# Kernel tuning notes

Hardware: AMD Instinct MI355X
Metric: run time of the kernel (lower is better)

Reference implementation:

```python
import jax, jax.numpy as jnp
import numpy as np
import math

P = 7          # patch / kernel size (must be odd for onion-peeling: N = 1+4*m*(m+1) = P*P)
EPS = 1e-6
EPS_W = 0.5

def _ball_dirs():
    u = [np.array([[1.0, 0.0]])]
    s = [np.zeros(1)]
    for k in range(1, P // 2 + 1):
        n = 8 * k
        th = np.linspace(0.0, 2.0 * math.pi * (1.0 - 1.0 / n), n)
        u.append(np.stack([np.cos(th), np.sin(th)], 1))
        s.append(np.full(n, k / (P // 2)))
    return (np.concatenate(u, 0).astype(np.float32), np.concatenate(s).astype(np.float32))

_U, _S = _ball_dirs()  # [N,2], [N], N == P*P == 49

def _forward(x, metric_w, metric_b, proj_w, proj_b):
    B, C, H, W = x.shape
    Hp, Wp = H // P, W // P
    u = jnp.asarray(_U)
    s = jnp.asarray(_S)
    # metric net: strided conv -> 7 params per patch
    params = jax.lax.conv_general_dilated(
        x, metric_w, (P, P), 'VALID',
        dimension_numbers=('NCHW', 'OIHW', 'NCHW')) + metric_b[None, :, None, None]
    v_raw = jnp.moveaxis(params[:, :2], 1, -1)                      # [B,Hp,Wp,2]
    v = v_raw / jnp.maximum(jnp.linalg.norm(v_raw, axis=-1, keepdims=True), 1e-12)
    eig = 2.0 * jax.nn.sigmoid(jnp.moveaxis(params[:, 2:4], 1, -1))  # [B,Hp,Wp,2]
    scale = 0.5 + 1.5 * jax.nn.sigmoid(jnp.moveaxis(params[:, 4:5], 1, -1))
    eig = eig * scale
    vp = jnp.stack([-v[..., 1], v[..., 0]], -1)
    R = jnp.stack([v, vp], -1)                                      # [B,Hp,Wp,2,2] (columns v, v_perp)
    M = R @ (eig[..., None] * jnp.swapaxes(R, -1, -2))              # R diag(eig) R^T
    w = params[:, 5:7]                                              # [B,2,Hp,Wp]
    w = w * (1.0 - EPS_W) * jax.nn.sigmoid(jnp.linalg.norm(w, axis=1, keepdims=True))
    # Finsler-Randers norm F(u) = sqrt(u^T M u + eps) + w.u for all N unit dirs
    quad = jnp.einsum('nj,bhwij,ni->bnhw', u, M, u)                 # [B,N,Hp,Wp]
    drift = jnp.einsum('bihw,ni->bnhw', w, u)
    F_u = jnp.sqrt(quad + EPS) + drift
    y = (u[None, :, :, None, None] / (F_u[:, :, None] + EPS)
         * s[None, :, None, None, None])                            # [B,N,2,Hp,Wp]
    y = y.reshape(B, P, P, 2, Hp, Wp)[:, :, :, ::-1]                # flip last coord pair (x,y)->(y,x)
    gi = jnp.arange(P, dtype=x.dtype) - P // 2
    grid = jnp.stack(jnp.meshgrid(gi, gi, indexing='ij'), -1)       # [P,P,2]
    off = y - grid[None, :, :, :, None, None]                       # [B,P,P,2,Hp,Wp]
    off_y = jnp.transpose(off[:, :, :, 0], (0, 3, 4, 1, 2))         # [B,Hp,Wp,P,P]
    off_x = jnp.transpose(off[:, :, :, 1], (0, 3, 4, 1, 2))
    base_h = (jnp.arange(Hp, dtype=x.dtype) * P)[None, :, None, None, None]
    base_w = (jnp.arange(Wp, dtype=x.dtype) * P)[None, None, :, None, None]
    ki = jnp.arange(P, dtype=x.dtype)
    py = off_y + base_h + ki[None, None, None, :, None]             # sample rows
    px = off_x + base_w + ki[None, None, None, None, :]             # sample cols
    # bilinear sampling with zero padding (torchvision deform_conv2d semantics)
    y0 = jnp.floor(py)
    x0 = jnp.floor(px)
    wy = py - y0
    wx = px - x0

    def gather(yi, xi):
        valid = (yi >= 0) & (yi <= H - 1) & (xi >= 0) & (xi <= W - 1)
        yc = jnp.clip(yi, 0, H - 1).astype(jnp.int32)
        xc = jnp.clip(xi, 0, W - 1).astype(jnp.int32)
        vals = jax.vmap(lambda img, yy, xx: img[:, yy, xx])(x, yc, xc)  # [B,C,Hp,Wp,P,P]
        return vals * valid[:, None].astype(x.dtype)

    sampled = (gather(y0, x0) * ((1 - wy) * (1 - wx))[:, None]
               + gather(y0, x0 + 1) * ((1 - wy) * wx)[:, None]
               + gather(y0 + 1, x0) * (wy * (1 - wx))[:, None]
               + gather(y0 + 1, x0 + 1) * (wy * wx)[:, None])       # [B,C,Hp,Wp,P,P]
    out = jnp.einsum('bchwij,ecij->behw', sampled, proj_w) + proj_b[None, :, None, None]
    return jnp.moveaxis(out.reshape(B, out.shape[1], -1), 1, 2)     # [B, Hp*Wp, E]

def setup_inputs():
    key = jax.random.key(0)
    k0, k1, k2 = jax.random.split(key, 3)
    B, C, H, W, E = 64, 3, 224, 224, 384
    x = jax.random.normal(k0, (B, C, H, W), jnp.float32)
    metric_w = jax.random.normal(k1, (7, C, P, P), jnp.float32) / math.sqrt(C * P * P)
    metric_b = jnp.zeros((7,), jnp.float32)
    proj_w = jax.random.normal(k2, (E, C, P, P), jnp.float32) / (P * math.sqrt(C))
    proj_b = jnp.zeros((E,), jnp.float32)
    return {"x": x, "metric_w": metric_w, "metric_b": metric_b,
            "proj_w": proj_w, "proj_b": proj_b}

def reference(x, metric_w, metric_b, proj_w, proj_b):
    return _forward(x, metric_w, metric_b, proj_w, proj_b)
```

## Files before the change

kernel.cpp:

```cpp
#include <hip/hip_runtime.h>
#include <math.h>

#define PP   7
#define NDIR 49
#define CIN  3
#define KK   147
#define KPAD 160
#define EE   384
#define HH   224
#define WW   224
#define GG   16
#define TB1  256
#define TB2  256
#define SSTR 17

typedef __attribute__((ext_vector_type(8))) __bf16 bf16x8;
typedef __attribute__((ext_vector_type(4))) float  f32x4;

__device__ __forceinline__ float sigmoidf_(float v) {
    return 1.0f / (1.0f + expf(-v));
}

__global__ void pack_pw_kernel(const float* __restrict__ pw, unsigned short* __restrict__ pwB) {
    int idx = blockIdx.x * blockDim.x + threadIdx.x;
    if (idx < EE * KPAD) {
        int e = idx / KPAD;
        int k = idx - e * KPAD;
        float v = (k < KK) ? pw[e * KK + k] : 0.0f;
        __bf16 h = (__bf16)v;
        pwB[idx] = *(unsigned short*)&h;
    }
}

__launch_bounds__(TB1)
__global__ void params_kernel(const float* __restrict__ x,
                              const float* __restrict__ mw,
                              const float* __restrict__ mb,
                              float* __restrict__ der) {
    __shared__ float mws[7 * KK];
    const int t = threadIdx.x;
    for (int i = t; i < 7 * KK; i += TB1) mws[i] = mw[i];
    __syncthreads();

    const int p   = blockIdx.x * TB1 + t;
    const int b   = p >> 10;
    const int rem = p & 1023;
    const int hp  = rem >> 5;
    const int wp  = rem & 31;
    const float* xb = x + (size_t)b * (CIN * HH * WW) + (size_t)(hp * PP) * WW + wp * PP;

    float a0 = mb[0], a1 = mb[1], a2 = mb[2], a3 = mb[3], a4 = mb[4], a5 = mb[5], a6 = mb[6];
    #pragma unroll
    for (int c = 0; c < CIN; ++c) {
        #pragma unroll
        for (int i = 0; i < PP; ++i) {
            const float* row = xb + c * (HH * WW) + i * WW;
            float v[7];
            #pragma unroll
            for (int j = 0; j < PP; ++j) v[j] = row[j];
            const int kb = c * 49 + i * 7;
            #pragma unroll
            for (int j = 0; j < PP; ++j) {
                a0 = fmaf(v[j], mws[0 * KK + kb + j], a0);
                a1 = fmaf(v[j], mws[1 * KK + kb + j], a1);
                a2 = fmaf(v[j], mws[2 * KK + kb + j], a2);
                a3 = fmaf(v[j], mws[3 * KK + kb + j], a3);
                a4 = fmaf(v[j], mws[4 * KK + kb + j], a4);
                a5 = fmaf(v[j], mws[5 * KK + kb + j], a5);
                a6 = fmaf(v[j], mws[6 * KK + kb + j], a6);
            }
        }
    }

    float nrm = sqrtf(a0 * a0 + a1 * a1);
    float inv = 1.0f / fmaxf(nrm, 1e-12f);
    float v0 = a0 * inv, v1 = a1 * inv;
    float e0 = 2.0f * sigmoidf_(a2);
    float e1 = 2.0f * sigmoidf_(a3);
    float sc = 0.5f + 1.5f * sigmoidf_(a4);
    e0 *= sc; e1 *= sc;
    float M00 = e0 * v0 * v0 + e1 * v1 * v1;
    float M01 = (e0 - e1) * v0 * v1;
    float M11 = e0 * v1 * v1 + e1 * v0 * v0;
    float wn  = sqrtf(a5 * a5 + a6 * a6);
    float wsc = 0.5f * sigmoidf_(wn);

    float* dp = der + (size_t)p * 8;
    dp[0] = M00; dp[1] = M01; dp[2] = M11; dp[3] = a5 * wsc; dp[4] = a6 * wsc;
}

__launch_bounds__(TB2)
__global__ void gather_gemm_kernel(const float* __restrict__ x,
                                   const float* __restrict__ derg,
                                   const unsigned short* __restrict__ pwB,
                                   const float* __restrict__ pb,
                                   float* __restrict__ out) {
    __shared__ float der_s[GG][5];
    __shared__ float dirs[NDIR][3];
    __shared__ float samp[KK][SSTR];

    const int t   = threadIdx.x;
    const int blk = blockIdx.x;
    const int b   = blk >> 6;
    const int rem = blk & 63;
    const int hp  = rem >> 1;
    const int wp0 = (rem & 1) * GG;
    const size_t m0 = (size_t)blk * GG;

    const float* xb = x + (size_t)b * (CIN * HH * WW);

    if (t < GG * 5) {
        int g = t / 5, f = t - g * 5;
        der_s[g][f] = derg[(m0 + g) * 8 + f];
    }
    if (t >= 64 && t < 64 + NDIR) {
        int n = t - 64;
        float u0, u1, s;
        if (n == 0)      { u0 = 1.0f; u1 = 0.0f; s = 0.0f; }
        else if (n < 9)  { float th = (float)(n - 1)  * 0.78539816339744831f; u0 = cosf(th); u1 = sinf(th); s = 0.33333334f; }
        else if (n < 25) { float th = (float)(n - 9)  * 0.39269908169872414f; u0 = cosf(th); u1 = sinf(th); s = 0.66666669f; }
        else             { float th = (float)(n - 25) * 0.26179938779914941f; u0 = cosf(th); u1 = sinf(th); s = 1.0f; }
        dirs[n][0] = u0; dirs[n][1] = u1; dirs[n][2] = s;
    }
    __syncthreads();

    for (int item = t; item < GG * NDIR; item += TB2) {
        int g = item / NDIR;
        int n = item - g * NDIR;
        float u0 = dirs[n][0], u1 = dirs[n][1], s = dirs[n][2];
        float M00 = der_s[g][0], M01 = der_s[g][1], M11 = der_s[g][2];
        float w0 = der_s[g][3], w1 = der_s[g][4];
        float quad  = u0 * u0 * M00 + 2.0f * u0 * u1 * M01 + u1 * u1 * M11;
        float drift = w0 * u0 + w1 * u1;
        float F = sqrtf(quad + 1e-6f) + drift;
        float r = s / (F + 1e-6f);
        float py = (float)(hp * PP + 3) + u1 * r;
        float px = (float)((wp0 + g) * PP + 3) + u0 * r;
        float y0f = floorf(py), x0f = floorf(px);
        float y1f = y0f + 1.0f, x1f = x0f + 1.0f;
        float wy = py - y0f, wx = px - x0f;
        bool vy0 = (y0f >= 0.0f) && (y0f <= (float)(HH - 1));
        bool vy1 = (y1f >= 0.0f) && (y1f <= (float)(HH - 1));
        bool vx0 = (x0f >= 0.0f) && (x0f <= (float)(WW - 1));
        bool vx1 = (x1f >= 0.0f) && (x1f <= (float)(WW - 1));
        int iy0 = (int)fminf(fmaxf(y0f, 0.0f), (float)(HH - 1));
        int iy1 = (int)fminf(fmaxf(y1f, 0.0f), (float)(HH - 1));
        int ix0 = (int)fminf(fmaxf(x0f, 0.0f), (float)(WW - 1));
        int ix1 = (int)fminf(fmaxf(x1f, 0.0f), (float)(WW - 1));
        float w00 = (1.0f - wy) * (1.0f - wx);
        float w01 = (1.0f - wy) * wx;
        float w10 = wy * (1.0f - wx);
        float w11 = wy * wx;
        #pragma unroll
        for (int c = 0; c < CIN; ++c) {
            const float* xc = xb + c * (HH * WW);
            float v00 = (vy0 && vx0) ? xc[iy0 * WW + ix0] : 0.0f;
            float v01 = (vy0 && vx1) ? xc[iy0 * WW + ix1] : 0.0f;
            float v10 = (vy1 && vx0) ? xc[iy1 * WW + ix0] : 0.0f;
            float v11 = (vy1 && vx1) ? xc[iy1 * WW + ix1] : 0.0f;
            samp[c * NDIR + n][g] = v00 * w00 + v01 * w01 + v10 * w10 + v11 * w11;
        }
    }
    __syncthreads();

    const int lane = t & 63;
    const int wv   = t >> 6;
    const int nrow = lane & 15;
    const int hi   = lane >> 4;

    bf16x8 afr[5];
    #pragma unroll
    for (int ks = 0; ks < 5; ++ks) {
        #pragma unroll
        for (int j = 0; j < 8; ++j) {
            int k = ks * 32 + hi * 8 + j;
            float v = (k < KK) ? samp[k][nrow] : 0.0f;
            afr[ks][j] = (__bf16)v;
        }
    }

    #pragma unroll
    for (int q = 0; q < 6; ++q) {
        int tile = wv * 6 + q;
        int e    = tile * 16 + nrow;
        const unsigned short* brow = pwB + (size_t)e * KPAD + hi * 8;
        f32x4 acc = {0.0f, 0.0f, 0.0f, 0.0f};
        #pragma unroll
        for (int ks = 0; ks < 5; ++ks) {
            bf16x8 bfr = *(const bf16x8*)&brow[ks * 32];
            acc = __builtin_amdgcn_mfma_f32_16x16x32_bf16(afr[ks], bfr, acc, 0, 0, 0);
        }
        float bias = pb[e];
        #pragma unroll
        for (int r = 0; r < 4; ++r) {
            out[(m0 + hi * 4 + r) * EE + e] = acc[r] + bias;
        }
    }
}

extern "C" void kernel_launch(void* const* d_in, const int* in_sizes, int n_in,
                              void* d_out, int out_size, void* d_ws, size_t ws_size,
                              hipStream_t stream) {
    const float* x  = (const float*)d_in[0];
    const float* mw = (const float*)d_in[1];
    const float* mb = (const float*)d_in[2];
    const float* pw = (const float*)d_in[3];
    const float* pb = (const float*)d_in[4];
    float* out = (float*)d_out;
    float* der = (float*)d_ws;
    unsigned short* pwB = (unsigned short*)((char*)d_ws + (size_t)65536 * 8 * 4);

    const int B = in_sizes[0] / (CIN * HH * WW);
    const int NPATCH = B * 32 * 32;

    pack_pw_kernel<<<(EE * KPAD + 255) / 256, 256, 0, stream>>>(pw, pwB);
    params_kernel<<<NPATCH / TB1, TB1, 0, stream>>>(x, mw, mb, der);
    gather_gemm_kernel<<<B * 64, TB2, 0, stream>>>(x, der, pwB, pb, out);
}
```

Measured before the change: 201.3 us.

## Fuse metric-param conv into gather-GEMM kernel and gather from channel-packed image

Drops the separate params kernel. Each gather-GEMM block now stages its 7-row input strip in shared memory and computes the 7 metric parameters for its 16 patches there, so the per-patch parameter buffer never goes through global memory. When workspace allows, a pre-pass repacks x into an interleaved 4-channel layout, so each bilinear tap becomes one 16-byte load instead of three scattered loads. The cost is an extra full pass over the input (writing about 1.3x its size) and more shared memory per block, which may reduce occupancy.

```diff
diff --git a/kernel.cpp b/kernel.cpp
--- a/kernel.cpp
+++ b/kernel.cpp
@@ -10,9 +10,9 @@
 #define HH   224
 #define WW   224
 #define GG   16
-#define TB1  256
-#define TB2  256
+#define TB   256
 #define SSTR 17
+#define NPX  112
 
 typedef __attribute__((ext_vector_type(8))) __bf16 bf16x8;
 typedef __attribute__((ext_vector_type(4))) float  f32x4;
@@ -32,72 +32,34 @@
     }
 }
 
-__launch_bounds__(TB1)
-__global__ void params_kernel(const float* __restrict__ x,
-                              const float* __restrict__ mw,
-                              const float* __restrict__ mb,
-                              float* __restrict__ der) {
+__global__ void pack_x_kernel(const float* __restrict__ x, float* __restrict__ xp, int npix) {
+    int idx = blockIdx.x * blockDim.x + threadIdx.x;
+    if (idx >= npix) return;
+    int b = idx / (HH * WW);
+    int p = idx - b * (HH * WW);
+    const float* xb = x + (size_t)b * (CIN * HH * WW) + p;
+    f32x4 v;
+    v[0] = xb[0];
+    v[1] = xb[HH * WW];
+    v[2] = xb[2 * HH * WW];
+    v[3] = 0.0f;
+    *(f32x4*)(xp + (size_t)idx * 4) = v;
+}
+
+template<bool PACKED>
+__launch_bounds__(TB)
+__global__ void fused_kernel(const float* __restrict__ x,
+                             const float* __restrict__ xp,
+                             const float* __restrict__ mw,
+                             const float* __restrict__ mb,
+                             const unsigned short* __restrict__ pwB,
+                             const float* __restrict__ pb,
+                             float* __restrict__ out) {
     __shared__ float mws[7 * KK];
-    const int t = threadIdx.x;
-    for (int i = t; i < 7 * KK; i += TB1) mws[i] = mw[i];
-    __syncthreads();
-
-    const int p   = blockIdx.x * TB1 + t;
-    const int b   = p >> 10;
-    const int rem = p & 1023;
-    const int hp  = rem >> 5;
-    const int wp  = rem & 31;
-    const float* xb = x + (size_t)b * (CIN * HH * WW) + (size_t)(hp * PP) * WW + wp * PP;
-
-    float a0 = mb[0], a1 = mb[1], a2 = mb[2], a3 = mb[3], a4 = mb[4], a5 = mb[5], a6 = mb[6];
-    #pragma unroll
-    for (int c = 0; c < CIN; ++c) {
-        #pragma unroll
-        for (int i = 0; i < PP; ++i) {
-            const float* row = xb + c * (HH * WW) + i * WW;
-            float v[7];
-            #pragma unroll
-            for (int j = 0; j < PP; ++j) v[j] = row[j];
-            const int kb = c * 49 + i * 7;
-            #pragma unroll
-            for (int j = 0; j < PP; ++j) {
-                a0 = fmaf(v[j], mws[0 * KK + kb + j], a0);
-                a1 = fmaf(v[j], mws[1 * KK + kb + j], a1);
-                a2 = fmaf(v[j], mws[2 * KK + kb + j], a2);
-                a3 = fmaf(v[j], mws[3 * KK + kb + j], a3);
-                a4 = fmaf(v[j], mws[4 * KK + kb + j], a4);
-                a5 = fmaf(v[j], mws[5 * KK + kb + j], a5);
-                a6 = fmaf(v[j], mws[6 * KK + kb + j], a6);
-            }
-        }
-    }
-
-    float nrm = sqrtf(a0 * a0 + a1 * a1);
-    float inv = 1.0f / fmaxf(nrm, 1e-12f);
-    float v0 = a0 * inv, v1 = a1 * inv;
-    float e0 = 2.0f * sigmoidf_(a2);
-    float e1 = 2.0f * sigmoidf_(a3);
-    float sc = 0.5f + 1.5f * sigmoidf_(a4);
-    e0 *= sc; e1 *= sc;
-    float M00 = e0 * v0 * v0 + e1 * v1 * v1;
-    float M01 = (e0 - e1) * v0 * v1;
-    float M11 = e0 * v1 * v1 + e1 * v0 * v0;
-    float wn  = sqrtf(a5 * a5 + a6 * a6);
-    float wsc = 0.5f * sigmoidf_(wn);
-
-    float* dp = der + (size_t)p * 8;
-    dp[0] = M00; dp[1] = M01; dp[2] = M11; dp[3] = a5 * wsc; dp[4] = a6 * wsc;
-}
-
-__launch_bounds__(TB2)
-__global__ void gather_gemm_kernel(const float* __restrict__ x,
-                                   const float* __restrict__ derg,
-                                   const unsigned short* __restrict__ pwB,
-                                   const float* __restrict__ pb,
-                                   float* __restrict__ out) {
+    __shared__ float dirs[NDIR][3];
+    __shared__ float par_s[GG][8];
     __shared__ float der_s[GG][5];
-    __shared__ float dirs[NDIR][3];
-    __shared__ float samp[KK][SSTR];
+    __shared__ float buf[3136];
 
     const int t   = threadIdx.x;
     const int blk = blockIdx.x;
@@ -106,13 +68,10 @@
     const int hp  = rem >> 1;
     const int wp0 = (rem & 1) * GG;
     const size_t m0 = (size_t)blk * GG;
-
-    const float* xb = x + (size_t)b * (CIN * HH * WW);
-
-    if (t < GG * 5) {
-        int g = t / 5, f = t - g * 5;
-        der_s[g][f] = derg[(m0 + g) * 8 + f];
-    }
+    const int row0 = hp * PP;
+    const int col0 = wp0 * PP;
+
+    for (int i = t; i < 7 * KK; i += TB) mws[i] = mw[i];
     if (t >= 64 && t < 64 + NDIR) {
         int n = t - 64;
         float u0, u1, s;
@@ -122,9 +81,66 @@
         else             { float th = (float)(n - 25) * 0.26179938779914941f; u0 = cosf(th); u1 = sinf(th); s = 1.0f; }
         dirs[n][0] = u0; dirs[n][1] = u1; dirs[n][2] = s;
     }
-    __syncthreads();
-
-    for (int item = t; item < GG * NDIR; item += TB2) {
+
+    if (PACKED) {
+        for (int item = t; item < 7 * NPX; item += TB) {
+            int i = item / NPX, px = item - i * NPX;
+            f32x4 v = *(const f32x4*)(xp + ((size_t)((b * HH + row0 + i) * WW) + col0 + px) * 4);
+            *(f32x4*)&buf[item * 4] = v;
+        }
+    } else {
+        for (int item = t; item < CIN * 7 * NPX; item += TB) {
+            int c = item / (7 * NPX), r2 = item - c * (7 * NPX);
+            int i = r2 / NPX, px = r2 - i * NPX;
+            buf[item] = x[(size_t)b * (CIN * HH * WW) + (size_t)c * (HH * WW)
+                          + (size_t)(row0 + i) * WW + col0 + px];
+        }
+    }
+    __syncthreads();
+
+    if (t < 112) {
+        int prm = t >> 4, g = t & 15;
+        float acc = mb[prm];
+        const float* wrow = &mws[prm * KK];
+        #pragma unroll
+        for (int c = 0; c < CIN; ++c) {
+            #pragma unroll
+            for (int i = 0; i < 7; ++i) {
+                #pragma unroll
+                for (int j = 0; j < 7; ++j) {
+                    float xv = PACKED ? buf[(i * NPX + g * 7 + j) * 4 + c]
+                                      : buf[(c * 7 + i) * NPX + g * 7 + j];
+                    acc = fmaf(xv, wrow[c * 49 + i * 7 + j], acc);
+                }
+            }
+        }
+        par_s[g][prm] = acc;
+    }
+    __syncthreads();
+
+    if (t < GG) {
+        float a0 = par_s[t][0], a1 = par_s[t][1], a2 = par_s[t][2], a3 = par_s[t][3];
+        float a4 = par_s[t][4], a5 = par_s[t][5], a6 = par_s[t][6];
+        float nrm = sqrtf(a0 * a0 + a1 * a1);
+        float inv = 1.0f / fmaxf(nrm, 1e-12f);
+        float v0 = a0 * inv, v1 = a1 * inv;
+        float e0 = 2.0f * sigmoidf_(a2);
+        float e1 = 2.0f * sigmoidf_(a3);
+        float sc = 0.5f + 1.5f * sigmoidf_(a4);
+        e0 *= sc; e1 *= sc;
+        float wn  = sqrtf(a5 * a5 + a6 * a6);
+        float wsc = 0.5f * sigmoidf_(wn);
+        der_s[t][0] = e0 * v0 * v0 + e1 * v1 * v1;
+        der_s[t][1] = (e0 - e1) * v0 * v1;
+        der_s[t][2] = e0 * v1 * v1 + e1 * v0 * v0;
+        der_s[t][3] = a5 * wsc;
+        der_s[t][4] = a6 * wsc;
+    }
+    __syncthreads();
+
+    const float* xb = x + (size_t)b * (CIN * HH * WW);
+    const size_t pbase = (size_t)b * (HH * WW);
+    for (int item = t; item < GG * NDIR; item += TB) {
         int g = item / NDIR;
         int n = item - g * NDIR;
         float u0 = dirs[n][0], u1 = dirs[n][1], s = dirs[n][2];
@@ -134,8 +150,8 @@
         float drift = w0 * u0 + w1 * u1;
         float F = sqrtf(quad + 1e-6f) + drift;
         float r = s / (F + 1e-6f);
-        float py = (float)(hp * PP + 3) + u1 * r;
-        float px = (float)((wp0 + g) * PP + 3) + u0 * r;
+        float py = (float)(row0 + 3) + u1 * r;
+        float px = (float)(col0 + g * PP + 3) + u0 * r;
         float y0f = floorf(py), x0f = floorf(px);
         float y1f = y0f + 1.0f, x1f = x0f + 1.0f;
         float wy = py - y0f, wx = px - x0f;
@@ -151,14 +167,31 @@
         float w01 = (1.0f - wy) * wx;
         float w10 = wy * (1.0f - wx);
         float w11 = wy * wx;
-        #pragma unroll
-        for (int c = 0; c < CIN; ++c) {
-            const float* xc = xb + c * (HH * WW);
-            float v00 = (vy0 && vx0) ? xc[iy0 * WW + ix0] : 0.0f;
-            float v01 = (vy0 && vx1) ? xc[iy0 * WW + ix1] : 0.0f;
-            float v10 = (vy1 && vx0) ? xc[iy1 * WW + ix0] : 0.0f;
-            float v11 = (vy1 && vx1) ? xc[iy1 * WW + ix1] : 0.0f;
-            samp[c * NDIR + n][g] = v00 * w00 + v01 * w01 + v10 * w10 + v11 * w11;
+        if (PACKED) {
+            float c00 = w00 * ((vy0 && vx0) ? 1.0f : 0.0f);
+            float c01 = w01 * ((vy0 && vx1) ? 1.0f : 0.0f);
+            float c10 = w10 * ((vy1 && vx0) ? 1.0f : 0.0f);
+            float c11 = w11 * ((vy1 && vx1) ? 1.0f : 0.0f);
+            f32x4 q00 = *(const f32x4*)(xp + (pbase + (size_t)(iy0 * WW + ix0)) * 4);
+            f32x4 q01 = *(const f32x4*)(xp + (pbase + (size_t)(iy0 * WW + ix1)) * 4);
+            f32x4 q10 = *(const f32x4*)(xp + (pbase + (size_t)(iy1 * WW + ix0)) * 4);
+            f32x4 q11 = *(const f32x4*)(xp + (pbase + (size_t)(iy1 * WW + ix1)) * 4);
+            #pragma unroll
+            for (int c = 0; c < CIN; ++c) {
+                buf[(c * NDIR + n) * SSTR + g] =
+                    q00[c] * c00 + q01[c] * c01 + q10[c] * c10 + q11[c] * c11;
+            }
+        } else {
+            #pragma unroll
+            for (int c = 0; c < CIN; ++c) {
+                const float* xc = xb + c * (HH * WW);
+                float v00 = (vy0 && vx0) ? xc[iy0 * WW + ix0] : 0.0f;
+                float v01 = (vy0 && vx1) ? xc[iy0 * WW + ix1] : 0.0f;
+                float v10 = (vy1 && vx0) ? xc[iy1 * WW + ix0] : 0.0f;
+                float v11 = (vy1 && vx1) ? xc[iy1 * WW + ix1] : 0.0f;
+                buf[(c * NDIR + n) * SSTR + g] =
+                    v00 * w00 + v01 * w01 + v10 * w10 + v11 * w11;
+            }
         }
     }
     __syncthreads();
@@ -174,7 +207,7 @@
         #pragma unroll
         for (int j = 0; j < 8; ++j) {
             int k = ks * 32 + hi * 8 + j;
-            float v = (k < KK) ? samp[k][nrow] : 0.0f;
+            float v = (k < KK) ? buf[k * SSTR + nrow] : 0.0f;
             afr[ks][j] = (__bf16)v;
         }
     }
@@ -207,13 +240,20 @@
     const float* pw = (const float*)d_in[3];
     const float* pb = (const float*)d_in[4];
     float* out = (float*)d_out;
-    float* der = (float*)d_ws;
-    unsigned short* pwB = (unsigned short*)((char*)d_ws + (size_t)65536 * 8 * 4);
+
+    unsigned short* pwB = (unsigned short*)d_ws;
+    float* xp = (float*)((char*)d_ws + (size_t)(1 << 17));
 
     const int B = in_sizes[0] / (CIN * HH * WW);
-    const int NPATCH = B * 32 * 32;
+    const int npix = B * HH * WW;
+    const size_t need = (size_t)(1 << 17) + (size_t)npix * 4 * sizeof(float);
+    const bool packed = ws_size >= need;
 
     pack_pw_kernel<<<(EE * KPAD + 255) / 256, 256, 0, stream>>>(pw, pwB);
-    params_kernel<<<NPATCH / TB1, TB1, 0, stream>>>(x, mw, mb, der);
-    gather_gemm_kernel<<<B * 64, TB2, 0, stream>>>(x, der, pwB, pb, out);
-}
+    if (packed) {
+        pack_x_kernel<<<(npix + 255) / 256, 256, 0, stream>>>(x, xp, npix);
+        fused_kernel<true><<<B * 64, TB, 0, stream>>>(x, xp, mw, mb, pwB, pb, out);
+    } else {
+        fused_kernel<false><<<B * 64, TB, 0, stream>>>(x, xp, mw, mb, pwB, pb, out);
+    }
+}
```

Result: slower. 235.7 us (+17.1%).
